# Kernel optimization log

Hardware: AMD Instinct MI355X
Metric: run time of the kernel (lower is better)

The kernel has to match this reference:

```python
import jax, jax.numpy as jnp
import numpy as np

B, C, H, W = 8, 64, 64, 64
T, G, HID = 8, 8, 64


def setup_inputs() -> dict:
    key = jax.random.key(0)
    ks = jax.random.split(key, 8)
    s = 0.05
    return {
        "h": jax.random.normal(ks[0], (B, C, H, W), jnp.float32),
        "w_in": jax.random.normal(ks[1], (G * T, C), jnp.float32) * s,
        "b_in": jnp.zeros((G * T,), jnp.float32),
        "w_ih": jax.random.normal(ks[2], (4 * HID, 1), jnp.float32) * s,
        "w_hh": jax.random.normal(ks[3], (4 * HID, HID), jnp.float32) * s,
        "b_ih": jnp.zeros((4 * HID,), jnp.float32),
        "b_hh": jnp.zeros((4 * HID,), jnp.float32),
        "w_s": jax.random.normal(ks[4], (1, HID), jnp.float32) * s,
        "b_s": jnp.zeros((1,), jnp.float32),
        "w_out": jax.random.normal(ks[5], (C, G * T), jnp.float32) * s,
        "b_out": jnp.zeros((C,), jnp.float32),
    }


def reference(h, w_in, b_in, w_ih, w_hh, b_ih, b_hh, w_s, b_s, w_out, b_out):
    Bb, Cc, Hh, Ww = h.shape
    # 1x1 conv in-projection: (B,C,H,W) -> (B,G*T,H,W)
    y = jnp.einsum('bchw,oc->bohw', h, w_in) + b_in[None, :, None, None]
    y = y.reshape(Bb, G, T, Hh, Ww)
    # (B,G,H,W,T) -> (N,T) scalar sequences
    seq = jnp.transpose(y, (0, 1, 3, 4, 2)).reshape(-1, T)
    N = seq.shape[0]
    xs = seq.T  # (T, N) time-major for scan
    bias = b_ih + b_hh  # (4H,)
    w_x = w_ih[:, 0]    # (4H,) scalar-input weights

    def step(carry, x_t):
        hprev, cprev = carry
        # gates: i, f, g, o in torch LSTM ordering
        gates = x_t[:, None] * w_x[None, :] + hprev @ w_hh.T + bias  # (N,4H)
        i, f, g, o = jnp.split(gates, 4, axis=1)
        i = jax.nn.sigmoid(i)
        f = jax.nn.sigmoid(f)
        o = jax.nn.sigmoid(o)
        g = jnp.tanh(g)
        c = f * cprev + i * g
        hn = o * jnp.tanh(c)
        s_t = hn @ w_s[0] + b_s[0]  # fused to_scalar: (N,)
        return (hn, c), s_t

    init = (jnp.zeros((N, HID), h.dtype), jnp.zeros((N, HID), h.dtype))
    _, s = jax.lax.scan(step, init, xs)  # s: (T, N)

    out = s.T.reshape(Bb, G, Hh, Ww, T)
    out = jnp.transpose(out, (0, 1, 4, 2, 3)).reshape(Bb, G * T, Hh, Ww)
    # 1x1 conv out-projection back to C channels
    out = jnp.einsum('bchw,oc->bohw', out, w_out) + b_out[None, :, None, None]
    return out
```

## Files before the change

### kernel.cpp

```cpp
#include <hip/hip_runtime.h>
#include <hip/hip_bf16.h>

#define HW    4096
#define BB    8
#define TT    8

constexpr int OFF_WFRAG = 0;
constexpr int OFF_WTOUT = OFF_WFRAG + 8704;
constexpr int OFF_WXB   = OFF_WTOUT + 4096;

typedef _Float16 halfx8 __attribute__((ext_vector_type(8)));
typedef float    floatx4 __attribute__((ext_vector_type(4)));
typedef float    floatx2 __attribute__((ext_vector_type(2)));

__device__ inline float fast_exp2(float x) {
#if __has_builtin(__builtin_amdgcn_exp2f)
    return __builtin_amdgcn_exp2f(x);
#else
    return __builtin_exp2f(x);
#endif
}
__device__ inline float fast_rcp(float x) {
#if __has_builtin(__builtin_amdgcn_rcpf)
    return __builtin_amdgcn_rcpf(x);
#else
    return 1.0f / x;
#endif
}
__device__ inline floatx2 exp2x2(floatx2 x) {
    floatx2 r; r.x = fast_exp2(x.x); r.y = fast_exp2(x.y); return r;
}
__device__ inline floatx2 rcpx2(floatx2 x) {
    floatx2 r; r.x = fast_rcp(x.x); r.y = fast_rcp(x.y); return r;
}
__device__ inline floatx2 fsig2(floatx2 x) {
    return rcpx2(exp2x2(x * -1.44269504088896f) + 1.0f);
}
__device__ inline floatx2 ftanh2(floatx2 x) {
    floatx2 r = rcpx2(exp2x2(x * 2.88539008177793f) + 1.0f);
    return r * -2.0f + 1.0f;
}

union pack8 { _Float16 h[8]; uint4 u; };

__global__ __launch_bounds__(256) void prep_kernel(
    const float* __restrict__ w_ih,  const float* __restrict__ w_hh,
    const float* __restrict__ b_ih,  const float* __restrict__ b_hh,
    const float* __restrict__ w_s,   const float* __restrict__ w_out,
    float* __restrict__ ws_f) {
    int tid = threadIdx.x;
    if (blockIdx.x == 0) {
        uint4* wf = (uint4*)(ws_f + OFF_WFRAG);
        #pragma unroll
        for (int i = 0; i < 8; ++i) {
            int e  = tid + 256 * i;
            int l  = e & 63;
            int fi = e >> 6;
            int nb = fi >> 1, kc = fi & 1;
            int gate = (l & 15) + 16 * nb;
            int hid  = kc * 32 + (l >> 4) * 8;
            const float* src = w_hh + gate * 64 + hid;
            pack8 p;
            #pragma unroll
            for (int j = 0; j < 8; ++j) p.h[j] = (_Float16)src[j];
            wf[e] = p.u;
        }
        if (tid < 128) {
            int l = tid & 63, kc = tid >> 6;
            pack8 p;
            #pragma unroll
            for (int j = 0; j < 8; ++j) p.h[j] = (_Float16)0.0f;
            if ((l & 15) == 0) {
                #pragma unroll
                for (int j = 0; j < 8; ++j)
                    p.h[j] = (_Float16)w_s[kc * 32 + (l >> 4) * 8 + j];
            }
            wf[2048 + kc * 64 + l] = p.u;
        }
    } else {
        #pragma unroll
        for (int i = 0; i < 16; ++i) {
            int idx = tid + 256 * i;
            int o = idx & 63, c = idx >> 6;
            ws_f[OFF_WTOUT + idx] = w_out[o * 64 + c];
        }
        floatx2* wxb = (floatx2*)(ws_f + OFF_WXB);
        floatx2 v; v.x = w_ih[tid]; v.y = b_ih[tid] + b_hh[tid];
        wxb[tid] = v;
    }
}

__global__ __launch_bounds__(512) void lstm_kernel(
    const float* __restrict__ hin,
    const float* __restrict__ ws_f,
    float* __restrict__ out,
    const float* __restrict__ w_in,
    const float* __restrict__ b_in,
    const float* __restrict__ b_s_p,
    const float* __restrict__ b_out) {
    __shared__ uint4 wfrag_lds[2176];
    __shared__ floatx2 wxb_lds[256];
    __shared__ __align__(16) float x_lds[1024];
    __shared__ __align__(16) _Float16 h_lds[9216];
    __shared__ __align__(16) float stile[1024];
    __shared__ __align__(16) float wt_lds[4096];

    int tid = threadIdx.x;
    int ptile = blockIdx.x & 255;
    int b     = blockIdx.x >> 8;
    int p0 = ptile * 16;

    int lane = tid & 63;
    int wv   = tid >> 6;
    int g    = wv;
    int s    = lane & 15;
    int q    = lane >> 4;

    const uint4* wfg = (const uint4*)(ws_f + OFF_WFRAG);
    #pragma unroll
    for (int i = 0; i < 5; ++i) {
        int e = tid + 512 * i;
        if (e < 2176) wfrag_lds[e] = wfg[e];
    }
    if (tid < 256) wxb_lds[tid] = ((const floatx2*)(ws_f + OFF_WXB))[tid];
    #pragma unroll
    for (int i = 0; i < 2; ++i)
        ((floatx4*)wt_lds)[tid + 512 * i] = ((const floatx4*)w_in)[tid + 512 * i];
    if (tid < 256) {
        int cc = tid >> 2, f4 = tid & 3;
        ((floatx4*)stile)[tid] = *(const floatx4*)&hin[(b * 64 + cc) * HW + p0 + f4 * 4];
    }
    __syncthreads();

    {
        floatx2 xacc; xacc.x = b_in[g * 8 + q]; xacc.y = b_in[g * 8 + q + 4];
        #pragma unroll 8
        for (int cc = 0; cc < 64; ++cc) {
            float hv = stile[cc * 16 + s];
            floatx2 w;
            w.x = wt_lds[(g * 8 + q) * 64 + cc];
            w.y = wt_lds[(g * 8 + q + 4) * 64 + cc];
            floatx2 h2; h2.x = hv; h2.y = hv;
            xacc = xacc + w * h2;
        }
        x_lds[g * 128 + q * 16 + s]       = xacc.x;
        x_lds[g * 128 + (q + 4) * 16 + s] = xacc.y;
    }
    #pragma unroll
    for (int i = 0; i < 9; ++i)
        ((unsigned*)h_lds)[tid + 512 * i] = 0u;
    __syncthreads();

    #pragma unroll
    for (int i = 0; i < 2; ++i)
        ((floatx4*)wt_lds)[tid + 512 * i] =
            ((const floatx4*)(ws_f + OFF_WTOUT))[tid + 512 * i];

    _Float16* hrow = h_lds + wv * 16 * 72;
    float bs = b_s_p[0];

    float c_st[4][4];
    #pragma unroll
    for (int hb = 0; hb < 4; ++hb)
        #pragma unroll
        for (int r = 0; r < 4; ++r) c_st[hb][r] = 0.0f;

    for (int t = 0; t < TT; ++t) {
        asm volatile("" ::: "memory");

        halfx8 a0 = *(const halfx8*)(hrow + s * 72 + q * 8);
        halfx8 a1 = *(const halfx8*)(hrow + s * 72 + q * 8 + 32);

        if (t > 0) {
            halfx8 sb0 = *(const halfx8*)&wfrag_lds[32 * 64 + lane];
            halfx8 sb1 = *(const halfx8*)&wfrag_lds[33 * 64 + lane];
            floatx4 sa = {0.f, 0.f, 0.f, 0.f};
            sa = __builtin_amdgcn_mfma_f32_16x16x32_f16(a0, sb0, sa, 0, 0, 0);
            sa = __builtin_amdgcn_mfma_f32_16x16x32_f16(a1, sb1, sa, 0, 0, 0);
            if (s == 0) {
                floatx4 o4 = {sa[0] + bs, sa[1] + bs, sa[2] + bs, sa[3] + bs};
                *(floatx4*)&stile[(g * 8 + (t - 1)) * 16 + q * 4] = o4;
            }
        }

        floatx4 xv = *(const floatx4*)&x_lds[g * 128 + t * 16 + q * 4];
        floatx2 xlo; xlo.x = xv[0]; xlo.y = xv[1];
        floatx2 xhi; xhi.x = xv[2]; xhi.y = xv[3];

        #pragma unroll
        for (int hb = 0; hb < 4; ++hb) {
            floatx4 acc[4];
            #pragma unroll
            for (int gi = 0; gi < 4; ++gi) {
                int nb = hb + 4 * gi;
                floatx2 wb = wxb_lds[s + 16 * nb];
                floatx2 lo = xlo * wb.x + wb.y;
                floatx2 hi = xhi * wb.x + wb.y;
                floatx4 a = {lo.x, lo.y, hi.x, hi.y};
                halfx8 b0 = *(const halfx8*)&wfrag_lds[(nb * 2 + 0) * 64 + lane];
                halfx8 b1 = *(const halfx8*)&wfrag_lds[(nb * 2 + 1) * 64 + lane];
                a = __builtin_amdgcn_mfma_f32_16x16x32_f16(a0, b0, a, 0, 0, 0);
                a = __builtin_amdgcn_mfma_f32_16x16x32_f16(a1, b1, a, 0, 0, 0);
                acc[gi] = a;
            }
            int s16 = s + 16 * hb;
            _Float16* wp = hrow + (q * 4) * 72 + s16;
            #pragma unroll
            for (int p = 0; p < 2; ++p) {
                int r0 = 2 * p;
                floatx2 iv; iv.x = acc[0][r0]; iv.y = acc[0][r0 + 1]; iv = fsig2(iv);
                floatx2 fv; fv.x = acc[1][r0]; fv.y = acc[1][r0 + 1]; fv = fsig2(fv);
                floatx2 gv; gv.x = acc[2][r0]; gv.y = acc[2][r0 + 1]; gv = ftanh2(gv);
                floatx2 ov; ov.x = acc[3][r0]; ov.y = acc[3][r0 + 1]; ov = fsig2(ov);
                floatx2 cp; cp.x = c_st[hb][r0]; cp.y = c_st[hb][r0 + 1];
                floatx2 c = fv * cp + iv * gv;
                c_st[hb][r0] = c.x; c_st[hb][r0 + 1] = c.y;
                floatx2 hn = ov * ftanh2(c);
                wp[(r0 + 0) * 72] = (_Float16)hn.x;
                wp[(r0 + 1) * 72] = (_Float16)hn.y;
            }
        }
    }
    {
        asm volatile("" ::: "memory");
        halfx8 a0 = *(const halfx8*)(hrow + s * 72 + q * 8);
        halfx8 a1 = *(const halfx8*)(hrow + s * 72 + q * 8 + 32);
        halfx8 sb0 = *(const halfx8*)&wfrag_lds[32 * 64 + lane];
        halfx8 sb1 = *(const halfx8*)&wfrag_lds[33 * 64 + lane];
        floatx4 sa = {0.f, 0.f, 0.f, 0.f};
        sa = __builtin_amdgcn_mfma_f32_16x16x32_f16(a0, sb0, sa, 0, 0, 0);
        sa = __builtin_amdgcn_mfma_f32_16x16x32_f16(a1, sb1, sa, 0, 0, 0);
        if (s == 0) {
            floatx4 o4 = {sa[0] + bs, sa[1] + bs, sa[2] + bs, sa[3] + bs};
            *(floatx4*)&stile[(g * 8 + 7) * 16 + q * 4] = o4;
        }
    }
    __syncthreads();

    {
        int px = tid & 15;
        int oo = tid >> 4;
        floatx2 acc; acc.x = b_out[oo]; acc.y = b_out[oo + 32];
        #pragma unroll 8
        for (int c = 0; c < 64; ++c) {
            float sv = stile[c * 16 + px];
            floatx2 w;
            w.x = wt_lds[c * 64 + oo];
            w.y = wt_lds[c * 64 + oo + 32];
            floatx2 s2; s2.x = sv; s2.y = sv;
            acc = acc + w * s2;
        }
        out[(b * 64 + oo) * HW + p0 + px]      = acc.x;
        out[(b * 64 + oo + 32) * HW + p0 + px] = acc.y;
    }
}

extern "C" void kernel_launch(void* const* d_in, const int* in_sizes, int n_in,
                              void* d_out, int out_size, void* d_ws, size_t ws_size,
                              hipStream_t stream) {
    const float* h     = (const float*)d_in[0];
    const float* w_in  = (const float*)d_in[1];
    const float* b_in  = (const float*)d_in[2];
    const float* w_ih  = (const float*)d_in[3];
    const float* w_hh  = (const float*)d_in[4];
    const float* b_ih  = (const float*)d_in[5];
    const float* b_hh  = (const float*)d_in[6];
    const float* w_s   = (const float*)d_in[7];
    const float* b_s   = (const float*)d_in[8];
    const float* w_out = (const float*)d_in[9];
    const float* b_out = (const float*)d_in[10];
    float* out = (float*)d_out;
    float* ws  = (float*)d_ws;

    prep_kernel<<<2, 256, 0, stream>>>(w_ih, w_hh, b_ih, b_hh, w_s, w_out, ws);
    lstm_kernel<<<2048, 512, 0, stream>>>(h, ws, out, w_in, b_in, b_s, b_out);
}
```

Baseline: 244.8 us.

## Fold weight prep into LSTM kernel and batch gate reciprocals

Removes the separate prep kernel launch. Every block now converts w_hh to fp16 MFMA fragments and loads w_in/w_out into a padded (stride 65) LDS layout itself. The gate nonlinearities now share one reciprocal per group of four denominators through a product trick, which cuts rcp instructions at the cost of extra multiplies and some overflow risk when exp2 values get large. The trade is one fewer launch in exchange for redundant per-block weight conversion and strided global reads of w_out.

Result: slower. 250.3 us (+2.2%).

```diff
diff --git a/kernel.cpp b/kernel.cpp
--- a/kernel.cpp
+++ b/kernel.cpp
@@ -4,10 +4,6 @@
 #define HW    4096
 #define BB    8
 #define TT    8
-
-constexpr int OFF_WFRAG = 0;
-constexpr int OFF_WTOUT = OFF_WFRAG + 8704;
-constexpr int OFF_WXB   = OFF_WTOUT + 4096;
 
 typedef _Float16 halfx8 __attribute__((ext_vector_type(8)));
 typedef float    floatx4 __attribute__((ext_vector_type(4)));
@@ -33,77 +29,28 @@
 __device__ inline floatx2 rcpx2(floatx2 x) {
     floatx2 r; r.x = fast_rcp(x.x); r.y = fast_rcp(x.y); return r;
 }
-__device__ inline floatx2 fsig2(floatx2 x) {
-    return rcpx2(exp2x2(x * -1.44269504088896f) + 1.0f);
-}
-__device__ inline floatx2 ftanh2(floatx2 x) {
-    floatx2 r = rcpx2(exp2x2(x * 2.88539008177793f) + 1.0f);
-    return r * -2.0f + 1.0f;
-}
 
 union pack8 { _Float16 h[8]; uint4 u; };
-
-__global__ __launch_bounds__(256) void prep_kernel(
-    const float* __restrict__ w_ih,  const float* __restrict__ w_hh,
-    const float* __restrict__ b_ih,  const float* __restrict__ b_hh,
-    const float* __restrict__ w_s,   const float* __restrict__ w_out,
-    float* __restrict__ ws_f) {
-    int tid = threadIdx.x;
-    if (blockIdx.x == 0) {
-        uint4* wf = (uint4*)(ws_f + OFF_WFRAG);
-        #pragma unroll
-        for (int i = 0; i < 8; ++i) {
-            int e  = tid + 256 * i;
-            int l  = e & 63;
-            int fi = e >> 6;
-            int nb = fi >> 1, kc = fi & 1;
-            int gate = (l & 15) + 16 * nb;
-            int hid  = kc * 32 + (l >> 4) * 8;
-            const float* src = w_hh + gate * 64 + hid;
-            pack8 p;
-            #pragma unroll
-            for (int j = 0; j < 8; ++j) p.h[j] = (_Float16)src[j];
-            wf[e] = p.u;
-        }
-        if (tid < 128) {
-            int l = tid & 63, kc = tid >> 6;
-            pack8 p;
-            #pragma unroll
-            for (int j = 0; j < 8; ++j) p.h[j] = (_Float16)0.0f;
-            if ((l & 15) == 0) {
-                #pragma unroll
-                for (int j = 0; j < 8; ++j)
-                    p.h[j] = (_Float16)w_s[kc * 32 + (l >> 4) * 8 + j];
-            }
-            wf[2048 + kc * 64 + l] = p.u;
-        }
-    } else {
-        #pragma unroll
-        for (int i = 0; i < 16; ++i) {
-            int idx = tid + 256 * i;
-            int o = idx & 63, c = idx >> 6;
-            ws_f[OFF_WTOUT + idx] = w_out[o * 64 + c];
-        }
-        floatx2* wxb = (floatx2*)(ws_f + OFF_WXB);
-        floatx2 v; v.x = w_ih[tid]; v.y = b_ih[tid] + b_hh[tid];
-        wxb[tid] = v;
-    }
-}
 
 __global__ __launch_bounds__(512) void lstm_kernel(
     const float* __restrict__ hin,
-    const float* __restrict__ ws_f,
-    float* __restrict__ out,
     const float* __restrict__ w_in,
     const float* __restrict__ b_in,
+    const float* __restrict__ w_ih,
+    const float* __restrict__ w_hh,
+    const float* __restrict__ b_ih,
+    const float* __restrict__ b_hh,
+    const float* __restrict__ w_s,
     const float* __restrict__ b_s_p,
-    const float* __restrict__ b_out) {
+    const float* __restrict__ w_out,
+    const float* __restrict__ b_out,
+    float* __restrict__ out) {
     __shared__ uint4 wfrag_lds[2176];
     __shared__ floatx2 wxb_lds[256];
     __shared__ __align__(16) float x_lds[1024];
     __shared__ __align__(16) _Float16 h_lds[9216];
     __shared__ __align__(16) float stile[1024];
-    __shared__ __align__(16) float wt_lds[4096];
+    __shared__ float wt_lds[4160];
 
     int tid = threadIdx.x;
     int ptile = blockIdx.x & 255;
@@ -116,16 +63,44 @@
     int s    = lane & 15;
     int q    = lane >> 4;
 
-    const uint4* wfg = (const uint4*)(ws_f + OFF_WFRAG);
-    #pragma unroll
-    for (int i = 0; i < 5; ++i) {
-        int e = tid + 512 * i;
-        if (e < 2176) wfrag_lds[e] = wfg[e];
-    }
-    if (tid < 256) wxb_lds[tid] = ((const floatx2*)(ws_f + OFF_WXB))[tid];
-    #pragma unroll
-    for (int i = 0; i < 2; ++i)
-        ((floatx4*)wt_lds)[tid + 512 * i] = ((const floatx4*)w_in)[tid + 512 * i];
+    #pragma unroll
+    for (int i = 0; i < 4; ++i) {
+        int e  = tid + 512 * i;
+        int l  = e & 63;
+        int fi = e >> 6;
+        int nb = fi >> 1, kc = fi & 1;
+        int gate = (l & 15) + 16 * nb;
+        int hid  = kc * 32 + (l >> 4) * 8;
+        const floatx4* src = (const floatx4*)&w_hh[gate * 64 + hid];
+        floatx4 v0 = src[0], v1 = src[1];
+        pack8 p;
+        p.h[0] = (_Float16)v0[0]; p.h[1] = (_Float16)v0[1];
+        p.h[2] = (_Float16)v0[2]; p.h[3] = (_Float16)v0[3];
+        p.h[4] = (_Float16)v1[0]; p.h[5] = (_Float16)v1[1];
+        p.h[6] = (_Float16)v1[2]; p.h[7] = (_Float16)v1[3];
+        wfrag_lds[e] = p.u;
+    }
+    if (tid < 128) {
+        int l = tid & 63, kc = tid >> 6;
+        pack8 p;
+        #pragma unroll
+        for (int j = 0; j < 8; ++j) p.h[j] = (_Float16)0.0f;
+        if ((l & 15) == 0) {
+            #pragma unroll
+            for (int j = 0; j < 8; ++j)
+                p.h[j] = (_Float16)w_s[kc * 32 + (l >> 4) * 8 + j];
+        }
+        wfrag_lds[2048 + kc * 64 + l] = p.u;
+    }
+    if (tid < 256) {
+        floatx2 v; v.x = w_ih[tid]; v.y = b_ih[tid] + b_hh[tid];
+        wxb_lds[tid] = v;
+    }
+    #pragma unroll
+    for (int i = 0; i < 8; ++i) {
+        int idx = tid + 512 * i;
+        wt_lds[(idx >> 6) * 65 + (idx & 63)] = w_in[idx];
+    }
     if (tid < 256) {
         int cc = tid >> 2, f4 = tid & 3;
         ((floatx4*)stile)[tid] = *(const floatx4*)&hin[(b * 64 + cc) * HW + p0 + f4 * 4];
@@ -138,8 +113,8 @@
         for (int cc = 0; cc < 64; ++cc) {
             float hv = stile[cc * 16 + s];
             floatx2 w;
-            w.x = wt_lds[(g * 8 + q) * 64 + cc];
-            w.y = wt_lds[(g * 8 + q + 4) * 64 + cc];
+            w.x = wt_lds[(g * 8 + q) * 65 + cc];
+            w.y = wt_lds[(g * 8 + q + 4) * 65 + cc];
             floatx2 h2; h2.x = hv; h2.y = hv;
             xacc = xacc + w * h2;
         }
@@ -152,12 +127,16 @@
     __syncthreads();
 
     #pragma unroll
-    for (int i = 0; i < 2; ++i)
-        ((floatx4*)wt_lds)[tid + 512 * i] =
-            ((const floatx4*)(ws_f + OFF_WTOUT))[tid + 512 * i];
+    for (int i = 0; i < 8; ++i) {
+        int idx = tid + 512 * i;
+        wt_lds[(idx >> 6) * 65 + (idx & 63)] = w_out[idx];
+    }
 
     _Float16* hrow = h_lds + wv * 16 * 72;
     float bs = b_s_p[0];
+
+    const float KS = -1.44269504088896f;
+    const float KT =  2.88539008177793f;
 
     float c_st[4][4];
     #pragma unroll
@@ -172,8 +151,8 @@
         halfx8 a1 = *(const halfx8*)(hrow + s * 72 + q * 8 + 32);
 
         if (t > 0) {
-            halfx8 sb0 = *(const halfx8*)&wfrag_lds[32 * 64 + lane];
-            halfx8 sb1 = *(const halfx8*)&wfrag_lds[33 * 64 + lane];
+            halfx8 sb0 = *(const halfx8*)&wfrag_lds[2048 + lane];
+            halfx8 sb1 = *(const halfx8*)&wfrag_lds[2112 + lane];
             floatx4 sa = {0.f, 0.f, 0.f, 0.f};
             sa = __builtin_amdgcn_mfma_f32_16x16x32_f16(a0, sb0, sa, 0, 0, 0);
             sa = __builtin_amdgcn_mfma_f32_16x16x32_f16(a1, sb1, sa, 0, 0, 0);
@@ -203,30 +182,53 @@
                 a = __builtin_amdgcn_mfma_f32_16x16x32_f16(a1, b1, a, 0, 0, 0);
                 acc[gi] = a;
             }
-            int s16 = s + 16 * hb;
-            _Float16* wp = hrow + (q * 4) * 72 + s16;
-            #pragma unroll
-            for (int p = 0; p < 2; ++p) {
-                int r0 = 2 * p;
-                floatx2 iv; iv.x = acc[0][r0]; iv.y = acc[0][r0 + 1]; iv = fsig2(iv);
-                floatx2 fv; fv.x = acc[1][r0]; fv.y = acc[1][r0 + 1]; fv = fsig2(fv);
-                floatx2 gv; gv.x = acc[2][r0]; gv.y = acc[2][r0 + 1]; gv = ftanh2(gv);
-                floatx2 ov; ov.x = acc[3][r0]; ov.y = acc[3][r0 + 1]; ov = fsig2(ov);
-                floatx2 cp; cp.x = c_st[hb][r0]; cp.y = c_st[hb][r0 + 1];
-                floatx2 c = fv * cp + iv * gv;
-                c_st[hb][r0] = c.x; c_st[hb][r0 + 1] = c.y;
-                floatx2 hn = ov * ftanh2(c);
-                wp[(r0 + 0) * 72] = (_Float16)hn.x;
-                wp[(r0 + 1) * 72] = (_Float16)hn.y;
-            }
+            #define ACCP(gi, p) (floatx2{acc[gi][2*(p)], acc[gi][2*(p)+1]})
+            floatx2 dI0 = exp2x2(ACCP(0,0) * KS) + 1.0f;
+            floatx2 dI1 = exp2x2(ACCP(0,1) * KS) + 1.0f;
+            floatx2 dF0 = exp2x2(ACCP(1,0) * KS) + 1.0f;
+            floatx2 dF1 = exp2x2(ACCP(1,1) * KS) + 1.0f;
+            floatx2 q1 = dI0 * dI1, q2 = q1 * dF0, q3 = q2 * dF1;
+            floatx2 R  = rcpx2(q3);
+            floatx2 fg1 = R * q2;  R = R * dF1;
+            floatx2 fg0 = R * q1;  R = R * dF0;
+            floatx2 ig1 = R * dI0;
+            floatx2 ig0 = R * dI1;
+            floatx2 dG0 = exp2x2(ACCP(2,0) * KT) + 1.0f;
+            floatx2 dG1 = exp2x2(ACCP(2,1) * KT) + 1.0f;
+            floatx2 dO0 = exp2x2(ACCP(3,0) * KS) + 1.0f;
+            floatx2 dO1 = exp2x2(ACCP(3,1) * KS) + 1.0f;
+            q1 = dG0 * dG1; q2 = q1 * dO0; q3 = q2 * dO1;
+            R  = rcpx2(q3);
+            floatx2 og1 = R * q2;  R = R * dO1;
+            floatx2 og0 = R * q1;  R = R * dO0;
+            floatx2 gv1 = (R * dG0) * -2.0f + 1.0f;
+            floatx2 gv0 = (R * dG1) * -2.0f + 1.0f;
+            floatx2 cp0; cp0.x = c_st[hb][0]; cp0.y = c_st[hb][1];
+            floatx2 cp1; cp1.x = c_st[hb][2]; cp1.y = c_st[hb][3];
+            floatx2 c0 = fg0 * cp0 + ig0 * gv0;
+            floatx2 c1 = fg1 * cp1 + ig1 * gv1;
+            c_st[hb][0] = c0.x; c_st[hb][1] = c0.y;
+            c_st[hb][2] = c1.x; c_st[hb][3] = c1.y;
+            floatx2 dc0 = exp2x2(c0 * KT) + 1.0f;
+            floatx2 dc1 = exp2x2(c1 * KT) + 1.0f;
+            floatx2 qc = dc0 * dc1;
+            floatx2 Rc = rcpx2(qc);
+            floatx2 h1 = og1 * ((Rc * dc0) * -2.0f + 1.0f);
+            floatx2 h0 = og0 * ((Rc * dc1) * -2.0f + 1.0f);
+            _Float16* wp = hrow + (q * 4) * 72 + s + 16 * hb;
+            wp[0 * 72] = (_Float16)h0.x;
+            wp[1 * 72] = (_Float16)h0.y;
+            wp[2 * 72] = (_Float16)h1.x;
+            wp[3 * 72] = (_Float16)h1.y;
+            #undef ACCP
         }
     }
     {
         asm volatile("" ::: "memory");
         halfx8 a0 = *(const halfx8*)(hrow + s * 72 + q * 8);
         halfx8 a1 = *(const halfx8*)(hrow + s * 72 + q * 8 + 32);
-        halfx8 sb0 = *(const halfx8*)&wfrag_lds[32 * 64 + lane];
-        halfx8 sb1 = *(const halfx8*)&wfrag_lds[33 * 64 + lane];
+        halfx8 sb0 = *(const halfx8*)&wfrag_lds[2048 + lane];
+        halfx8 sb1 = *(const halfx8*)&wfrag_lds[2112 + lane];
         floatx4 sa = {0.f, 0.f, 0.f, 0.f};
         sa = __builtin_amdgcn_mfma_f32_16x16x32_f16(a0, sb0, sa, 0, 0, 0);
         sa = __builtin_amdgcn_mfma_f32_16x16x32_f16(a1, sb1, sa, 0, 0, 0);
@@ -245,8 +247,8 @@
         for (int c = 0; c < 64; ++c) {
             float sv = stile[c * 16 + px];
             floatx2 w;
-            w.x = wt_lds[c * 64 + oo];
-            w.y = wt_lds[c * 64 + oo + 32];
+            w.x = wt_lds[oo * 65 + c];
+            w.y = wt_lds[(oo + 32) * 65 + c];
             floatx2 s2; s2.x = sv; s2.y = sv;
             acc = acc + w * s2;
         }
@@ -270,8 +272,8 @@
     const float* w_out = (const float*)d_in[9];
     const float* b_out = (const float*)d_in[10];
     float* out = (float*)d_out;
-    float* ws  = (float*)d_ws;
-
-    prep_kernel<<<2, 256, 0, stream>>>(w_ih, w_hh, b_ih, b_hh, w_s, w_out, ws);
-    lstm_kernel<<<2048, 512, 0, stream>>>(h, ws, out, w_in, b_in, b_s, b_out);
-}
+    (void)d_ws; (void)ws_size;
+
+    lstm_kernel<<<2048, 512, 0, stream>>>(h, w_in, b_in, w_ih, w_hh, b_ih, b_hh,
+                                          w_s, b_s, w_out, b_out, out);
+}
```

## Fold weight prep into single kernel with 20-pixel tiles and 10 waves per block

Applied to the files above, without the earlier changes.

Removes the separate prep kernel: each block converts w_hh/w_s to fp16 MFMA fragments and loads w_in/w_out directly into a padded (stride 65) LDS region that reuses the h-state buffer. Blocks now cover 20 pixels with 640 threads (10 waves), giving 205x8 blocks instead of 2048, which cuts per-block weight staging overhead and drops the wt_lds array. In exchange every block redundantly converts weights, uses non-power-of-two indexing with scalar stores, and leaves a partial last tile where some lanes compute padding.

Measured after the change: 342.8 us. +40.0%, slower.

```diff
diff --git a/kernel.cpp b/kernel.cpp
--- a/kernel.cpp
+++ b/kernel.cpp
@@ -2,12 +2,7 @@
 #include <hip/hip_bf16.h>
 
 #define HW    4096
-#define BB    8
 #define TT    8
-
-constexpr int OFF_WFRAG = 0;
-constexpr int OFF_WTOUT = OFF_WFRAG + 8704;
-constexpr int OFF_WXB   = OFF_WTOUT + 4096;
 
 typedef _Float16 halfx8 __attribute__((ext_vector_type(8)));
 typedef float    floatx4 __attribute__((ext_vector_type(4)));
@@ -43,118 +38,119 @@
 
 union pack8 { _Float16 h[8]; uint4 u; };
 
-__global__ __launch_bounds__(256) void prep_kernel(
-    const float* __restrict__ w_ih,  const float* __restrict__ w_hh,
-    const float* __restrict__ b_ih,  const float* __restrict__ b_hh,
-    const float* __restrict__ w_s,   const float* __restrict__ w_out,
-    float* __restrict__ ws_f) {
+__global__ __launch_bounds__(640) void lstm_kernel(
+    const float* __restrict__ hin,
+    const float* __restrict__ w_in,
+    const float* __restrict__ b_in,
+    const float* __restrict__ w_ih,
+    const float* __restrict__ w_hh,
+    const float* __restrict__ b_ih,
+    const float* __restrict__ b_hh,
+    const float* __restrict__ w_s,
+    const float* __restrict__ b_s_p,
+    const float* __restrict__ w_out,
+    const float* __restrict__ b_out,
+    float* __restrict__ out) {
+    __shared__ uint4 wfrag_lds[2176];
+    __shared__ floatx2 wxb_lds[256];
+    __shared__ __align__(16) float x_lds[1280];
+    __shared__ __align__(16) _Float16 h_lds[11520];
+    __shared__ __align__(16) float stile[1280];
+    float* hreg = (float*)h_lds;
+
     int tid = threadIdx.x;
-    if (blockIdx.x == 0) {
-        uint4* wf = (uint4*)(ws_f + OFF_WFRAG);
-        #pragma unroll
-        for (int i = 0; i < 8; ++i) {
-            int e  = tid + 256 * i;
+    int ptile = blockIdx.x;
+    int b     = blockIdx.y;
+    int p0  = ptile * 20;
+    int npx = (ptile == 204) ? 16 : 20;
+
+    int lane = tid & 63;
+    int wv   = tid >> 6;
+    int s    = lane & 15;
+    int q    = lane >> 4;
+
+    #pragma unroll
+    for (int i = 0; i < 4; ++i) {
+        int e = tid + 640 * i;
+        if (e < 2048) {
             int l  = e & 63;
             int fi = e >> 6;
             int nb = fi >> 1, kc = fi & 1;
             int gate = (l & 15) + 16 * nb;
             int hid  = kc * 32 + (l >> 4) * 8;
-            const float* src = w_hh + gate * 64 + hid;
+            const floatx4* src = (const floatx4*)&w_hh[gate * 64 + hid];
+            floatx4 v0 = src[0], v1 = src[1];
             pack8 p;
+            p.h[0] = (_Float16)v0[0]; p.h[1] = (_Float16)v0[1];
+            p.h[2] = (_Float16)v0[2]; p.h[3] = (_Float16)v0[3];
+            p.h[4] = (_Float16)v1[0]; p.h[5] = (_Float16)v1[1];
+            p.h[6] = (_Float16)v1[2]; p.h[7] = (_Float16)v1[3];
+            wfrag_lds[e] = p.u;
+        }
+    }
+    if (tid < 128) {
+        int l = tid & 63, kc = tid >> 6;
+        pack8 p;
+        #pragma unroll
+        for (int j = 0; j < 8; ++j) p.h[j] = (_Float16)0.0f;
+        if ((l & 15) == 0) {
             #pragma unroll
-            for (int j = 0; j < 8; ++j) p.h[j] = (_Float16)src[j];
-            wf[e] = p.u;
-        }
-        if (tid < 128) {
-            int l = tid & 63, kc = tid >> 6;
-            pack8 p;
-            #pragma unroll
-            for (int j = 0; j < 8; ++j) p.h[j] = (_Float16)0.0f;
-            if ((l & 15) == 0) {
-                #pragma unroll
-                for (int j = 0; j < 8; ++j)
-                    p.h[j] = (_Float16)w_s[kc * 32 + (l >> 4) * 8 + j];
-            }
-            wf[2048 + kc * 64 + l] = p.u;
-        }
-    } else {
-        #pragma unroll
-        for (int i = 0; i < 16; ++i) {
-            int idx = tid + 256 * i;
-            int o = idx & 63, c = idx >> 6;
-            ws_f[OFF_WTOUT + idx] = w_out[o * 64 + c];
-        }
-        floatx2* wxb = (floatx2*)(ws_f + OFF_WXB);
+            for (int j = 0; j < 8; ++j)
+                p.h[j] = (_Float16)w_s[kc * 32 + (l >> 4) * 8 + j];
+        }
+        wfrag_lds[2048 + kc * 64 + l] = p.u;
+    }
+    if (tid < 256) {
         floatx2 v; v.x = w_ih[tid]; v.y = b_ih[tid] + b_hh[tid];
-        wxb[tid] = v;
-    }
-}
-
-__global__ __launch_bounds__(512) void lstm_kernel(
-    const float* __restrict__ hin,
-    const float* __restrict__ ws_f,
-    float* __restrict__ out,
-    const float* __restrict__ w_in,
-    const float* __restrict__ b_in,
-    const float* __restrict__ b_s_p,
-    const float* __restrict__ b_out) {
-    __shared__ uint4 wfrag_lds[2176];
-    __shared__ floatx2 wxb_lds[256];
-    __shared__ __align__(16) float x_lds[1024];
-    __shared__ __align__(16) _Float16 h_lds[9216];
-    __shared__ __align__(16) float stile[1024];
-    __shared__ __align__(16) float wt_lds[4096];
-
-    int tid = threadIdx.x;
-    int ptile = blockIdx.x & 255;
-    int b     = blockIdx.x >> 8;
-    int p0 = ptile * 16;
-
-    int lane = tid & 63;
-    int wv   = tid >> 6;
-    int g    = wv;
-    int s    = lane & 15;
-    int q    = lane >> 4;
-
-    const uint4* wfg = (const uint4*)(ws_f + OFF_WFRAG);
-    #pragma unroll
-    for (int i = 0; i < 5; ++i) {
-        int e = tid + 512 * i;
-        if (e < 2176) wfrag_lds[e] = wfg[e];
-    }
-    if (tid < 256) wxb_lds[tid] = ((const floatx2*)(ws_f + OFF_WXB))[tid];
-    #pragma unroll
-    for (int i = 0; i < 2; ++i)
-        ((floatx4*)wt_lds)[tid + 512 * i] = ((const floatx4*)w_in)[tid + 512 * i];
-    if (tid < 256) {
-        int cc = tid >> 2, f4 = tid & 3;
-        ((floatx4*)stile)[tid] = *(const floatx4*)&hin[(b * 64 + cc) * HW + p0 + f4 * 4];
+        wxb_lds[tid] = v;
+    }
+    #pragma unroll
+    for (int i = 0; i < 7; ++i) {
+        int idx = tid + 640 * i;
+        if (idx < 4096) hreg[(idx >> 6) * 65 + (idx & 63)] = w_in[idx];
+    }
+    #pragma unroll
+    for (int i = 0; i < 2; ++i) {
+        int idx = tid + 640 * i;
+        if (idx < 1280) {
+            int cc = idx / 20, px = idx % 20;
+            stile[idx] = (px < npx) ? hin[(b * 64 + cc) * HW + p0 + px] : 0.0f;
+        }
     }
     __syncthreads();
 
     {
-        floatx2 xacc; xacc.x = b_in[g * 8 + q]; xacc.y = b_in[g * 8 + q + 4];
+        int px   = tid % 20;
+        int rest = tid / 20;
+        int tq = rest & 3, g = rest >> 2;
+        floatx2 xacc; xacc.x = b_in[g * 8 + tq]; xacc.y = b_in[g * 8 + tq + 4];
         #pragma unroll 8
         for (int cc = 0; cc < 64; ++cc) {
-            float hv = stile[cc * 16 + s];
+            float hv = stile[cc * 20 + px];
             floatx2 w;
-            w.x = wt_lds[(g * 8 + q) * 64 + cc];
-            w.y = wt_lds[(g * 8 + q + 4) * 64 + cc];
-            floatx2 h2; h2.x = hv; h2.y = hv;
-            xacc = xacc + w * h2;
-        }
-        x_lds[g * 128 + q * 16 + s]       = xacc.x;
-        x_lds[g * 128 + (q + 4) * 16 + s] = xacc.y;
-    }
-    #pragma unroll
-    for (int i = 0; i < 9; ++i)
-        ((unsigned*)h_lds)[tid + 512 * i] = 0u;
-    __syncthreads();
-
-    #pragma unroll
-    for (int i = 0; i < 2; ++i)
-        ((floatx4*)wt_lds)[tid + 512 * i] =
-            ((const floatx4*)(ws_f + OFF_WTOUT))[tid + 512 * i];
+            w.x = hreg[(g * 8 + tq) * 65 + cc];
+            w.y = hreg[(g * 8 + tq + 4) * 65 + cc];
+            xacc.x += w.x * hv;
+            xacc.y += w.y * hv;
+        }
+        x_lds[tq * 160 + g * 20 + px]       = xacc.x;
+        x_lds[(tq + 4) * 160 + g * 20 + px] = xacc.y;
+    }
+    __syncthreads();
+    #pragma unroll
+    for (int i = 0; i < 9; ++i) {
+        int idx = tid + 640 * i;
+        if (idx < 5760) ((unsigned*)h_lds)[idx] = 0u;
+    }
+    __syncthreads();
+
+    int sb[4];
+    #pragma unroll
+    for (int r = 0; r < 4; ++r) {
+        int sg = wv * 16 + q * 4 + r;
+        int gr = sg / 20, pxr = sg % 20;
+        sb[r] = gr * 160 + pxr;
+    }
 
     _Float16* hrow = h_lds + wv * 16 * 72;
     float bs = b_s_p[0];
@@ -172,18 +168,21 @@
         halfx8 a1 = *(const halfx8*)(hrow + s * 72 + q * 8 + 32);
 
         if (t > 0) {
-            halfx8 sb0 = *(const halfx8*)&wfrag_lds[32 * 64 + lane];
-            halfx8 sb1 = *(const halfx8*)&wfrag_lds[33 * 64 + lane];
+            halfx8 sb0 = *(const halfx8*)&wfrag_lds[2048 + lane];
+            halfx8 sb1 = *(const halfx8*)&wfrag_lds[2112 + lane];
             floatx4 sa = {0.f, 0.f, 0.f, 0.f};
             sa = __builtin_amdgcn_mfma_f32_16x16x32_f16(a0, sb0, sa, 0, 0, 0);
             sa = __builtin_amdgcn_mfma_f32_16x16x32_f16(a1, sb1, sa, 0, 0, 0);
             if (s == 0) {
-                floatx4 o4 = {sa[0] + bs, sa[1] + bs, sa[2] + bs, sa[3] + bs};
-                *(floatx4*)&stile[(g * 8 + (t - 1)) * 16 + q * 4] = o4;
+                int toff = (t - 1) * 20;
+                stile[sb[0] + toff] = sa[0] + bs;
+                stile[sb[1] + toff] = sa[1] + bs;
+                stile[sb[2] + toff] = sa[2] + bs;
+                stile[sb[3] + toff] = sa[3] + bs;
             }
         }
 
-        floatx4 xv = *(const floatx4*)&x_lds[g * 128 + t * 16 + q * 4];
+        floatx4 xv = *(const floatx4*)&x_lds[t * 160 + wv * 16 + q * 4];
         floatx2 xlo; xlo.x = xv[0]; xlo.y = xv[1];
         floatx2 xhi; xhi.x = xv[2]; xhi.y = xv[3];
 
@@ -225,33 +224,41 @@
         asm volatile("" ::: "memory");
         halfx8 a0 = *(const halfx8*)(hrow + s * 72 + q * 8);
         halfx8 a1 = *(const halfx8*)(hrow + s * 72 + q * 8 + 32);
-        halfx8 sb0 = *(const halfx8*)&wfrag_lds[32 * 64 + lane];
-        halfx8 sb1 = *(const halfx8*)&wfrag_lds[33 * 64 + lane];
+        halfx8 sb0 = *(const halfx8*)&wfrag_lds[2048 + lane];
+        halfx8 sb1 = *(const halfx8*)&wfrag_lds[2112 + lane];
         floatx4 sa = {0.f, 0.f, 0.f, 0.f};
         sa = __builtin_amdgcn_mfma_f32_16x16x32_f16(a0, sb0, sa, 0, 0, 0);
         sa = __builtin_amdgcn_mfma_f32_16x16x32_f16(a1, sb1, sa, 0, 0, 0);
         if (s == 0) {
-            floatx4 o4 = {sa[0] + bs, sa[1] + bs, sa[2] + bs, sa[3] + bs};
-            *(floatx4*)&stile[(g * 8 + 7) * 16 + q * 4] = o4;
-        }
+            stile[sb[0] + 140] = sa[0] + bs;
+            stile[sb[1] + 140] = sa[1] + bs;
+            stile[sb[2] + 140] = sa[2] + bs;
+            stile[sb[3] + 140] = sa[3] + bs;
+        }
+    }
+    __syncthreads();
+
+    #pragma unroll
+    for (int i = 0; i < 7; ++i) {
+        int idx = tid + 640 * i;
+        if (idx < 4096) hreg[(idx >> 6) * 65 + (idx & 63)] = w_out[idx];
     }
     __syncthreads();
 
     {
-        int px = tid & 15;
-        int oo = tid >> 4;
-        floatx2 acc; acc.x = b_out[oo]; acc.y = b_out[oo + 32];
+        int px = tid % 20;
+        int o  = tid / 20;
+        floatx2 acc; acc.x = b_out[o]; acc.y = b_out[o + 32];
         #pragma unroll 8
         for (int c = 0; c < 64; ++c) {
-            float sv = stile[c * 16 + px];
-            floatx2 w;
-            w.x = wt_lds[c * 64 + oo];
-            w.y = wt_lds[c * 64 + oo + 32];
-            floatx2 s2; s2.x = sv; s2.y = sv;
-            acc = acc + w * s2;
-        }
-        out[(b * 64 + oo) * HW + p0 + px]      = acc.x;
-        out[(b * 64 + oo + 32) * HW + p0 + px] = acc.y;
+            float sv = stile[c * 20 + px];
+            acc.x += hreg[o * 65 + c] * sv;
+            acc.y += hreg[(o + 32) * 65 + c] * sv;
+        }
+        if (px < npx) {
+            out[(b * 64 + o) * HW + p0 + px]      = acc.x;
+            out[(b * 64 + o + 32) * HW + p0 + px] = acc.y;
+        }
     }
 }
 
@@ -270,8 +277,9 @@
     const float* w_out = (const float*)d_in[9];
     const float* b_out = (const float*)d_in[10];
     float* out = (float*)d_out;
-    float* ws  = (float*)d_ws;
-
-    prep_kernel<<<2, 256, 0, stream>>>(w_ih, w_hh, b_ih, b_hh, w_s, w_out, ws);
-    lstm_kernel<<<2048, 512, 0, stream>>>(h, ws, out, w_in, b_in, b_s, b_out);
-}
+    (void)d_ws; (void)ws_size;
+
+    lstm_kernel<<<dim3(205, 8), 640, 0, stream>>>(h, w_in, b_in, w_ih, w_hh,
+                                                  b_ih, b_hh, w_s, b_s,
+                                                  w_out, b_out, out);
+}
```

## Alias projection weights into h_lds with padded rows to cut LDS footprint

Applied to the files above, without the earlier changes.

Removes the separate 16KB wt_lds buffer and stages w_in and later w_out in the h_lds region (which is idle before and after the recurrence) using a 65-float padded row stride. This lowers shared memory per block, which may allow more resident blocks per CU, and the padding is meant to avoid bank conflicts on the per-row weight reads. The w_out transpose in the prep kernel is dropped, so weights are loaded directly from global memory per block. In exchange it adds two extra barriers and uses scalar rather than vectorized global loads for the weight staging.

After: 245.9 us. No clear change (+0.4%).

```diff
diff --git a/kernel.cpp b/kernel.cpp
--- a/kernel.cpp
+++ b/kernel.cpp
@@ -2,12 +2,10 @@
 #include <hip/hip_bf16.h>
 
 #define HW    4096
-#define BB    8
 #define TT    8
 
 constexpr int OFF_WFRAG = 0;
-constexpr int OFF_WTOUT = OFF_WFRAG + 8704;
-constexpr int OFF_WXB   = OFF_WTOUT + 4096;
+constexpr int OFF_WXB   = 8704;
 
 typedef _Float16 halfx8 __attribute__((ext_vector_type(8)));
 typedef float    floatx4 __attribute__((ext_vector_type(4)));
@@ -46,8 +44,7 @@
 __global__ __launch_bounds__(256) void prep_kernel(
     const float* __restrict__ w_ih,  const float* __restrict__ w_hh,
     const float* __restrict__ b_ih,  const float* __restrict__ b_hh,
-    const float* __restrict__ w_s,   const float* __restrict__ w_out,
-    float* __restrict__ ws_f) {
+    const float* __restrict__ w_s,   float* __restrict__ ws_f) {
     int tid = threadIdx.x;
     if (blockIdx.x == 0) {
         uint4* wf = (uint4*)(ws_f + OFF_WFRAG);
@@ -78,12 +75,6 @@
             wf[2048 + kc * 64 + l] = p.u;
         }
     } else {
-        #pragma unroll
-        for (int i = 0; i < 16; ++i) {
-            int idx = tid + 256 * i;
-            int o = idx & 63, c = idx >> 6;
-            ws_f[OFF_WTOUT + idx] = w_out[o * 64 + c];
-        }
         floatx2* wxb = (floatx2*)(ws_f + OFF_WXB);
         floatx2 v; v.x = w_ih[tid]; v.y = b_ih[tid] + b_hh[tid];
         wxb[tid] = v;
@@ -93,21 +84,22 @@
 __global__ __launch_bounds__(512) void lstm_kernel(
     const float* __restrict__ hin,
     const float* __restrict__ ws_f,
-    float* __restrict__ out,
     const float* __restrict__ w_in,
     const float* __restrict__ b_in,
     const float* __restrict__ b_s_p,
-    const float* __restrict__ b_out) {
+    const float* __restrict__ w_out,
+    const float* __restrict__ b_out,
+    float* __restrict__ out) {
     __shared__ uint4 wfrag_lds[2176];
     __shared__ floatx2 wxb_lds[256];
     __shared__ __align__(16) float x_lds[1024];
     __shared__ __align__(16) _Float16 h_lds[9216];
     __shared__ __align__(16) float stile[1024];
-    __shared__ __align__(16) float wt_lds[4096];
+    float* hreg = (float*)h_lds;
 
     int tid = threadIdx.x;
-    int ptile = blockIdx.x & 255;
-    int b     = blockIdx.x >> 8;
+    int ptile = blockIdx.x;
+    int b     = blockIdx.y;
     int p0 = ptile * 16;
 
     int lane = tid & 63;
@@ -124,8 +116,10 @@
     }
     if (tid < 256) wxb_lds[tid] = ((const floatx2*)(ws_f + OFF_WXB))[tid];
     #pragma unroll
-    for (int i = 0; i < 2; ++i)
-        ((floatx4*)wt_lds)[tid + 512 * i] = ((const floatx4*)w_in)[tid + 512 * i];
+    for (int i = 0; i < 8; ++i) {
+        int idx = tid + 512 * i;
+        hreg[(idx >> 6) * 65 + (idx & 63)] = w_in[idx];
+    }
     if (tid < 256) {
         int cc = tid >> 2, f4 = tid & 3;
         ((floatx4*)stile)[tid] = *(const floatx4*)&hin[(b * 64 + cc) * HW + p0 + f4 * 4];
@@ -138,23 +132,19 @@
         for (int cc = 0; cc < 64; ++cc) {
             float hv = stile[cc * 16 + s];
             floatx2 w;
-            w.x = wt_lds[(g * 8 + q) * 64 + cc];
-            w.y = wt_lds[(g * 8 + q + 4) * 64 + cc];
-            floatx2 h2; h2.x = hv; h2.y = hv;
-            xacc = xacc + w * h2;
+            w.x = hreg[(g * 8 + q) * 65 + cc];
+            w.y = hreg[(g * 8 + q + 4) * 65 + cc];
+            xacc.x += w.x * hv;
+            xacc.y += w.y * hv;
         }
         x_lds[g * 128 + q * 16 + s]       = xacc.x;
         x_lds[g * 128 + (q + 4) * 16 + s] = xacc.y;
     }
+    __syncthreads();
     #pragma unroll
     for (int i = 0; i < 9; ++i)
         ((unsigned*)h_lds)[tid + 512 * i] = 0u;
     __syncthreads();
-
-    #pragma unroll
-    for (int i = 0; i < 2; ++i)
-        ((floatx4*)wt_lds)[tid + 512 * i] =
-            ((const floatx4*)(ws_f + OFF_WTOUT))[tid + 512 * i];
 
     _Float16* hrow = h_lds + wv * 16 * 72;
     float bs = b_s_p[0];
@@ -172,8 +162,8 @@
         halfx8 a1 = *(const halfx8*)(hrow + s * 72 + q * 8 + 32);
 
         if (t > 0) {
-            halfx8 sb0 = *(const halfx8*)&wfrag_lds[32 * 64 + lane];
-            halfx8 sb1 = *(const halfx8*)&wfrag_lds[33 * 64 + lane];
+            halfx8 sb0 = *(const halfx8*)&wfrag_lds[2048 + lane];
+            halfx8 sb1 = *(const halfx8*)&wfrag_lds[2112 + lane];
             floatx4 sa = {0.f, 0.f, 0.f, 0.f};
             sa = __builtin_amdgcn_mfma_f32_16x16x32_f16(a0, sb0, sa, 0, 0, 0);
             sa = __builtin_amdgcn_mfma_f32_16x16x32_f16(a1, sb1, sa, 0, 0, 0);
@@ -225,8 +215,8 @@
         asm volatile("" ::: "memory");
         halfx8 a0 = *(const halfx8*)(hrow + s * 72 + q * 8);
         halfx8 a1 = *(const halfx8*)(hrow + s * 72 + q * 8 + 32);
-        halfx8 sb0 = *(const halfx8*)&wfrag_lds[32 * 64 + lane];
-        halfx8 sb1 = *(const halfx8*)&wfrag_lds[33 * 64 + lane];
+        halfx8 sb0 = *(const halfx8*)&wfrag_lds[2048 + lane];
+        halfx8 sb1 = *(const halfx8*)&wfrag_lds[2112 + lane];
         floatx4 sa = {0.f, 0.f, 0.f, 0.f};
         sa = __builtin_amdgcn_mfma_f32_16x16x32_f16(a0, sb0, sa, 0, 0, 0);
         sa = __builtin_amdgcn_mfma_f32_16x16x32_f16(a1, sb1, sa, 0, 0, 0);
@@ -234,6 +224,13 @@
             floatx4 o4 = {sa[0] + bs, sa[1] + bs, sa[2] + bs, sa[3] + bs};
             *(floatx4*)&stile[(g * 8 + 7) * 16 + q * 4] = o4;
         }
+    }
+    __syncthreads();
+
+    #pragma unroll
+    for (int i = 0; i < 8; ++i) {
+        int idx = tid + 512 * i;
+        hreg[(idx >> 6) * 65 + (idx & 63)] = w_out[idx];
     }
     __syncthreads();
 
@@ -244,11 +241,8 @@
         #pragma unroll 8
         for (int c = 0; c < 64; ++c) {
             float sv = stile[c * 16 + px];
-            floatx2 w;
-            w.x = wt_lds[c * 64 + oo];
-            w.y = wt_lds[c * 64 + oo + 32];
-            floatx2 s2; s2.x = sv; s2.y = sv;
-            acc = acc + w * s2;
+            acc.x += hreg[oo * 65 + c] * sv;
+            acc.y += hreg[(oo + 32) * 65 + c] * sv;
         }
         out[(b * 64 + oo) * HW + p0 + px]      = acc.x;
         out[(b * 64 + oo + 32) * HW + p0 + px] = acc.y;
@@ -272,6 +266,7 @@
     float* out = (float*)d_out;
     float* ws  = (float*)d_ws;
 
-    prep_kernel<<<2, 256, 0, stream>>>(w_ih, w_hh, b_ih, b_hh, w_s, w_out, ws);
-    lstm_kernel<<<2048, 512, 0, stream>>>(h, ws, out, w_in, b_in, b_s, b_out);
-}
+    prep_kernel<<<2, 256, 0, stream>>>(w_ih, w_hh, b_ih, b_hh, w_s, ws);
+    lstm_kernel<<<dim3(256, 8), 512, 0, stream>>>(h, ws, w_in, b_in, b_s,
+                                                  w_out, b_out, out);
+}
```
